# Optimization experiments

Measured on AMD Instinct MI355X. Metric: run time of the kernel, lower is better.

Reference implementation:

```python
import jax, jax.numpy as jnp
import numpy as np

BZ, C, H, W = 8, 512, 64, 64


def setup_inputs() -> dict:
    key = jax.random.key(0)
    x = jax.random.normal(key, (BZ, C, H, W), dtype=jnp.float32)
    # central square hole: flag==1 -> masked (unknown), flag==0 -> known
    mask = np.zeros((H, W), dtype=np.int32)
    mask[H // 4: 3 * H // 4, W // 4: 3 * W // 4] = 1
    return {"x": x, "mask": jnp.asarray(mask)}


def reference(x, mask):
    # InnerShiftSingle forward with shift_sz=1, stride=1, mask_thred=1:
    # flag == feature-level mask (each 1x1 patch is masked iff its pixel is masked).
    bz, c, h, w = x.shape
    c2 = c // 2
    hw = h * w
    flag = mask.reshape(hw)  # [hw] int, 1=masked, 0=known

    former = x[:, :c2]   # decoder features [b,c2,h,w]
    latter = x[:, c2:]   # encoder features [b,c2,h,w]

    former_f = former.reshape(bz, c2, hw).transpose(0, 2, 1)  # [b,hw,c2]
    latter_f = latter.reshape(bz, c2, hw).transpose(0, 2, 1)  # [b,hw,c2]

    # original: conv of (un-normalized) former with L2-normalized latter 1x1 patches
    latter_n = latter_f / (jnp.linalg.norm(latter_f, axis=-1, keepdims=True) + 1e-8)
    cosine = jnp.einsum('bpc,bqc->bpq', former_f, latter_n)  # [b,hw,hw]
    # only known-region patches (flag==0) are candidate sources
    cosine = jnp.where(flag[None, None, :] == 1, -jnp.inf, cosine)

    best = jnp.argmax(cosine, axis=-1)  # [b,hw] index into known region
    shift = jnp.take_along_axis(latter_f, best[..., None], axis=1)  # [b,hw,c2]
    # only masked positions receive a shifted feature; known positions stay 0
    shift = jnp.where(flag[None, :, None] == 1, shift, jnp.zeros((), x.dtype))
    shift = shift.transpose(0, 2, 1).reshape(bz, c2, h, w)

    return jnp.concatenate([former, latter, shift], axis=1)  # [b, 3c/2, h, w]
```

## Files before the change

### kernel.cpp

```cpp
#include <hip/hip_runtime.h>
#include <math.h>

#define BZc 8
#define Cc 512
#define C2c 256
#define HWc 4096
#define OUTC 768
#define NP 1024
#define NQ 3072
#define QG 8
#define TAU 5e-5f
#define FIXSLOTS 64

typedef _Float16 h8 __attribute__((ext_vector_type(8)));
typedef float f16v __attribute__((ext_vector_type(16)));
typedef float f32x4 __attribute__((ext_vector_type(4)));

__global__ __launch_bounds__(1024) void k_build(const int* __restrict__ mask,
                                                int* __restrict__ pidx,
                                                int* __restrict__ qinv,
                                                int* __restrict__ pinv,
                                                int* __restrict__ cnt) {
    __shared__ int s0[1024], s1[1024], t0[1024], t1[1024];
    int t = threadIdx.x;
    if (t < 8) cnt[t] = 0;
    int f[4];
    int cp = 0;
#pragma unroll
    for (int j = 0; j < 4; ++j) { f[j] = mask[t * 4 + j]; cp += f[j]; }
    s0[t] = cp; s1[t] = 4 - cp;
    __syncthreads();
    int *a = s0, *b = s1, *c = t0, *d = t1;
    for (int off = 1; off < 1024; off <<= 1) {
        int vp = a[t] + (t >= off ? a[t - off] : 0);
        int vq = b[t] + (t >= off ? b[t - off] : 0);
        c[t] = vp; d[t] = vq;
        __syncthreads();
        int* tmp;
        tmp = a; a = c; c = tmp;
        tmp = b; b = d; d = tmp;
    }
    int ep = a[t] - cp;
    int eq = b[t] - (4 - cp);
#pragma unroll
    for (int j = 0; j < 4; ++j) {
        int idx = t * 4 + j;
        if (f[j]) { pidx[ep] = idx; pinv[idx] = ep; qinv[idx] = -1; ep++; }
        else      { qinv[idx] = eq; pinv[idx] = -1; eq++; }
    }
}

__global__ __launch_bounds__(256) void k_prep(const float* __restrict__ x,
                                              const int* __restrict__ pinv,
                                              const int* __restrict__ qinv,
                                              _Float16* __restrict__ latH,
                                              _Float16* __restrict__ latL,
                                              _Float16* __restrict__ forH,
                                              _Float16* __restrict__ forL,
                                              float* __restrict__ invn,
                                              float* __restrict__ invnC,
                                              float* __restrict__ out) {
    int id = blockIdx.x;
    bool isLat = id < 1024;
    int rid = isLat ? id : id - 1024;
    int b = rid >> 7;
    int g = rid & 127;
    int col0 = g * 32;
    int tid = threadIdx.x;
    __shared__ float tile[64][33];
    __shared__ float ssq[32][33];
    __shared__ int rowm[32];
    if (tid < 32) rowm[tid] = isLat ? qinv[col0 + tid] : pinv[col0 + tid];
    const float* xb = x + (size_t)b * Cc * HWc + (isLat ? (size_t)C2c * HWc : 0);
    float* ob = out + (size_t)b * OUTC * HWc + (isLat ? (size_t)C2c * HWc : 0);
    _Float16* dH = isLat ? latH + (size_t)b * NQ * 256 : forH + (size_t)b * NP * 256;
    _Float16* dL = isLat ? latL + (size_t)b * NQ * 256 : forL + (size_t)b * NP * 256;

    int cr = tid >> 3;
    int c4 = (tid & 7) * 4;

    f32x4 vv[4][2];
#pragma unroll
    for (int c = 0; c < 4; ++c) {
        vv[c][0] = *(const f32x4*)(xb + (size_t)(c * 64 + cr) * HWc + col0 + c4);
        vv[c][1] = *(const f32x4*)(xb + (size_t)(c * 64 + 32 + cr) * HWc + col0 + c4);
    }
    __syncthreads();

    int qq = tid >> 3, sub = tid & 7;
    int dr = rowm[qq];

#pragma unroll
    for (int c = 0; c < 4; ++c) {
        int ch0 = c * 64;
        {
            f32x4 v0 = vv[c][0], v1 = vv[c][1];
            tile[cr][c4]      = v0.x; tile[cr][c4 + 1]      = v0.y;
            tile[cr][c4 + 2]  = v0.z; tile[cr][c4 + 3]      = v0.w;
            tile[32 + cr][c4] = v1.x; tile[32 + cr][c4 + 1] = v1.y;
            tile[32 + cr][c4 + 2] = v1.z; tile[32 + cr][c4 + 3] = v1.w;
        }
        __syncthreads();
        if (dr >= 0) {
            h8 hv, lv;
#pragma unroll
            for (int j = 0; j < 8; ++j) {
                float v = tile[sub * 8 + j][qq];
                _Float16 h = (_Float16)v;
                hv[j] = h; lv[j] = (_Float16)((v - (float)h) * 2048.0f);
            }
            size_t o = (size_t)dr * 256 + ch0 + sub * 8;
            *(h8*)(dH + o) = hv;
            *(h8*)(dL + o) = lv;
        }
        __syncthreads();
    }

#pragma unroll
    for (int c = 0; c < 4; ++c) {
        *(f32x4*)(ob + (size_t)(c * 64 + cr) * HWc + col0 + c4) = vv[c][0];
        *(f32x4*)(ob + (size_t)(c * 64 + 32 + cr) * HWc + col0 + c4) = vv[c][1];
    }

    if (isLat) {
        float s0 = 0.f, s1 = 0.f, s2 = 0.f, s3 = 0.f;
#pragma unroll
        for (int c = 0; c < 4; ++c)
#pragma unroll
            for (int p = 0; p < 2; ++p) {
                f32x4 v = vv[c][p];
                s0 = fmaf(v.x, v.x, s0); s1 = fmaf(v.y, v.y, s1);
                s2 = fmaf(v.z, v.z, s2); s3 = fmaf(v.w, v.w, s3);
            }
        ssq[cr][c4] = s0; ssq[cr][c4 + 1] = s1; ssq[cr][c4 + 2] = s2; ssq[cr][c4 + 3] = s3;
        __syncthreads();
        if (tid < 32) {
            float s = 0.f;
#pragma unroll
            for (int r = 0; r < 32; ++r) s += ssq[r][tid];
            float inv = 1.0f / (sqrtf(s) + 1e-8f);
            invn[b * HWc + col0 + tid] = inv;
            int qc = rowm[tid];
            if (qc >= 0) invnC[b * NQ + qc] = inv;
        }
    } else {
        f32x4 z = {0.f, 0.f, 0.f, 0.f};
        float* sb = out + (size_t)b * OUTC * HWc + (size_t)Cc * HWc;
        for (int i = tid; i < 256 * 8; i += 256) {
            int ch = i >> 3, j4 = i & 7;
            *(f32x4*)(sb + (size_t)ch * HWc + col0 + j4 * 4) = z;
        }
    }
}

__global__ __launch_bounds__(512, 2) void k_gemm(const _Float16* __restrict__ latH,
                                                 const _Float16* __restrict__ latL,
                                                 const _Float16* __restrict__ forH,
                                                 const _Float16* __restrict__ forL,
                                                 const float* __restrict__ invnC,
                                                 float* __restrict__ bv1,
                                                 int* __restrict__ bi1,
                                                 float* __restrict__ bv2) {
    int pg = blockIdx.x;
    int qg = blockIdx.y;
    int b  = blockIdx.z;
    int tid = threadIdx.x;
    int w = tid >> 6, lane = tid & 63;
    int l31 = lane & 31, lh = lane >> 5;

    __shared__ __align__(16) _Float16 sH[2][32 * 256];
    __shared__ __align__(16) _Float16 sL[2][32 * 256];
    __shared__ float sInv[384];

    if (tid < 384) sInv[tid] = invnC[b * NQ + qg * 384 + tid];

    size_t fo = ((size_t)(b * NP + pg * 256 + w * 32 + l31)) * 256 + lh * 8;
    const _Float16* fH = forH + fo;
    const _Float16* fL = forL + fo;
    h8 BH[16], BL[16];
#pragma unroll
    for (int ks = 0; ks < 16; ++ks) {
        BH[ks] = *(const h8*)(fH + ks * 16);
        BL[ks] = *(const h8*)(fL + ks * 16);
    }

    const _Float16* latHb = latH + (size_t)(b * NQ + qg * 384) * 256;
    const _Float16* latLb = latL + (size_t)(b * NQ + qg * 384) * 256;
    int sq0 = tid >> 5;
    int sq1 = 16 + (tid >> 5);
    int ssl = tid & 31;

    float v1 = -INFINITY, v2 = -INFINITY; int i1 = 0;

    f32x4 rH0, rH1, rL0, rL1;
#define LOADQ(t)                                                                   \
    rH0 = *(const f32x4*)(latHb + ((size_t)((t) * 32 + sq0) * 256 + ssl * 8));     \
    rH1 = *(const f32x4*)(latHb + ((size_t)((t) * 32 + sq1) * 256 + ssl * 8));     \
    rL0 = *(const f32x4*)(latLb + ((size_t)((t) * 32 + sq0) * 256 + ssl * 8));     \
    rL1 = *(const f32x4*)(latLb + ((size_t)((t) * 32 + sq1) * 256 + ssl * 8));
#define WRITEQ(bf)                                                                 \
    *(f32x4*)(&sH[bf][sq0 * 256 + ((ssl ^ sq0) * 8)]) = rH0;                       \
    *(f32x4*)(&sH[bf][sq1 * 256 + ((ssl ^ sq1) * 8)]) = rH1;                       \
    *(f32x4*)(&sL[bf][sq0 * 256 + ((ssl ^ sq0) * 8)]) = rL0;                       \
    *(f32x4*)(&sL[bf][sq1 * 256 + ((ssl ^ sq1) * 8)]) = rL1;

    LOADQ(0); WRITEQ(0);
    __syncthreads();

    for (int t = 0; t < 12; ++t) {
        if (t < 11) { LOADQ(t + 1); }
        const _Float16* bufH = &sH[t & 1][0];
        const _Float16* bufL = &sL[t & 1][0];
        f16v accA = {}, accB = {};
#pragma unroll
        for (int ks = 0; ks < 16; ++ks) {
            int slotA = (ks * 2 + lh) ^ l31;
            h8 aH = *(const h8*)(bufH + l31 * 256 + slotA * 8);
            h8 aL = *(const h8*)(bufL + l31 * 256 + slotA * 8);
            accA = __builtin_amdgcn_mfma_f32_32x32x16_f16(aH, BH[ks], accA, 0, 0, 0);
            accB = __builtin_amdgcn_mfma_f32_32x32x16_f16(aH, BL[ks], accB, 0, 0, 0);
            accB = __builtin_amdgcn_mfma_f32_32x32x16_f16(aL, BH[ks], accB, 0, 0, 0);
        }
#pragma unroll
        for (int r = 0; r < 16; ++r) {
            int off = (r & 3) + 8 * (r >> 2) + 4 * lh;
            float v = (accA[r] + accB[r] * (1.0f / 2048.0f)) * sInv[t * 32 + off];
            int q = qg * 384 + t * 32 + off;
            if (v > v1) { v2 = v1; v1 = v; i1 = q; }
            else if (v > v2) { v2 = v; }
        }
        if (t < 11) { WRITEQ((t + 1) & 1); }
        __syncthreads();
    }
#undef LOADQ
#undef WRITEQ
    float ov1 = __shfl_xor(v1, 32);
    int   oi1 = __shfl_xor(i1, 32);
    float ov2 = __shfl_xor(v2, 32);
    if (ov1 > v1) { v2 = fmaxf(v1, ov2); v1 = ov1; i1 = oi1; }
    else          { v2 = fmaxf(ov1, v2); }
    if (lane < 32) {
        size_t o = ((size_t)b * NP + pg * 256 + w * 32 + lane) * QG + qg;
        bv1[o] = v1; bi1[o] = i1; bv2[o] = v2;
    }
}

__global__ void k_reduce(const float* __restrict__ bv1, const int* __restrict__ bi1,
                         const float* __restrict__ bv2, int* __restrict__ bfin,
                         int* __restrict__ cnt, int* __restrict__ fixrows) {
    int t = blockIdx.x * blockDim.x + threadIdx.x;
    if (t >= BZc * NP) return;
    float V1 = -INFINITY, V2 = -INFINITY; int I1 = 0;
    for (int c = 0; c < QG; ++c) {
        float a = bv1[(size_t)t * QG + c];
        float a2 = bv2[(size_t)t * QG + c];
        int   i = bi1[(size_t)t * QG + c];
        if (a > V1) { V2 = fmaxf(V1, a2); V1 = a; I1 = i; }
        else        { V2 = fmaxf(V2, a); }
    }
    bfin[t] = I1;
    if (V1 - V2 < TAU) {
        int b = t >> 10;
        int s = atomicAdd(&cnt[b], 1);
        if (s < FIXSLOTS) fixrows[b * FIXSLOTS + s] = t & 1023;
    }
}

__global__ __launch_bounds__(256) void k_fixA(const float* __restrict__ x,
                                              const int* __restrict__ pidx,
                                              const int* __restrict__ mask,
                                              const float* __restrict__ invn,
                                              const int* __restrict__ cnt,
                                              const int* __restrict__ fixrows,
                                              float* __restrict__ fixv,
                                              int* __restrict__ fixi) {
    int qg = blockIdx.x, s = blockIdx.y, b = blockIdx.z;
    int n = cnt[b]; if (n > FIXSLOTS) n = FIXSLOTS;
    if (s >= n) return;
    int p = fixrows[b * FIXSLOTS + s];
    int porig = pidx[p];
    int tid = threadIdx.x;
    __shared__ float fs[256];
    fs[tid] = x[((size_t)b * Cc + tid) * HWc + porig];
    __syncthreads();
    const float* lx = x + ((size_t)b * Cc + C2c) * HWc;
    int q0 = qg * 1024 + tid * 4;
    float4 acc = make_float4(0.f, 0.f, 0.f, 0.f);
    for (int c0 = 0; c0 < 256; c0 += 8) {
        float4 v[8];
#pragma unroll
        for (int u = 0; u < 8; ++u)
            v[u] = *(const float4*)(lx + (size_t)(c0 + u) * HWc + q0);
#pragma unroll
        for (int u = 0; u < 8; ++u) {
            float fc = fs[c0 + u];
            acc.x = fmaf(fc, v[u].x, acc.x);
            acc.y = fmaf(fc, v[u].y, acc.y);
            acc.z = fmaf(fc, v[u].z, acc.z);
            acc.w = fmaf(fc, v[u].w, acc.w);
        }
    }
    float vals[4] = {acc.x, acc.y, acc.z, acc.w};
    float bv = -INFINITY; int bq = 1 << 30;
#pragma unroll
    for (int k = 0; k < 4; ++k) {
        int q = q0 + k;
        float val = vals[k] * invn[b * HWc + q];
        if (mask[q] == 0 && val > bv) { bv = val; bq = q; }
    }
    __shared__ float rv[256]; __shared__ int rq[256];
    rv[tid] = bv; rq[tid] = bq; __syncthreads();
    for (int off = 128; off > 0; off >>= 1) {
        if (tid < off) {
            float v2 = rv[tid + off]; int q2 = rq[tid + off];
            if (v2 > rv[tid] || (v2 == rv[tid] && q2 < rq[tid])) { rv[tid] = v2; rq[tid] = q2; }
        }
        __syncthreads();
    }
    if (tid == 0) {
        fixv[(b * FIXSLOTS + s) * 4 + qg] = rv[0];
        fixi[(b * FIXSLOTS + s) * 4 + qg] = rq[0];
    }
}

__global__ void k_fixB(const int* __restrict__ cnt, const int* __restrict__ fixrows,
                       const float* __restrict__ fixv, const int* __restrict__ fixi,
                       const int* __restrict__ qinv, int* __restrict__ bfin) {
    int t = threadIdx.x;
    int b = t >> 6, s = t & 63;
    int n = cnt[b]; if (n > FIXSLOTS) n = FIXSLOTS;
    if (s >= n) return;
    float bv = -INFINITY; int bq = 1 << 30;
    for (int qg = 0; qg < 4; ++qg) {
        float v = fixv[(b * FIXSLOTS + s) * 4 + qg];
        int   q = fixi[(b * FIXSLOTS + s) * 4 + qg];
        if (v > bv || (v == bv && q < bq)) { bv = v; bq = q; }
    }
    int p = fixrows[b * FIXSLOTS + s];
    bfin[b * NP + p] = qinv[bq];
}

__global__ __launch_bounds__(256) void k_scatter(const _Float16* __restrict__ latH,
                                                 const _Float16* __restrict__ latL,
                                                 const int* __restrict__ bfin,
                                                 const int* __restrict__ pidx,
                                                 float* __restrict__ out) {
    int blk = blockIdx.x;
    int b   = blockIdx.y;
    int tid = threadIdx.x;
    __shared__ float tile[32][257];
    __shared__ int qd[32], pd[32];
    if (tid < 32) {
        qd[tid] = bfin[b * NP + blk * 32 + tid];
        pd[tid] = pidx[blk * 32 + tid];
    }
    __syncthreads();
    for (int i = tid; i < 32 * 256; i += 256) {
        int pp = i >> 8, c = i & 255;
        size_t o = ((size_t)b * NQ + qd[pp]) * 256 + c;
        tile[pp][c] = (float)latH[o] + (float)latL[o] * (1.0f / 2048.0f);
    }
    __syncthreads();
    float* ob = out + (size_t)b * OUTC * HWc + (size_t)Cc * HWc;
    for (int i = tid; i < 256 * 32; i += 256) {
        int ch = i >> 5, j = i & 31;
        ob[(size_t)ch * HWc + pd[j]] = tile[j][ch];
    }
}

extern "C" void kernel_launch(void* const* d_in, const int* in_sizes, int n_in,
                              void* d_out, int out_size, void* d_ws, size_t ws_size,
                              hipStream_t stream) {
    const float* x    = (const float*)d_in[0];
    const int*   mask = (const int*)d_in[1];
    float* out = (float*)d_out;
    char*  ws  = (char*)d_ws;

    _Float16* latH = (_Float16*)(ws);
    _Float16* latL = (_Float16*)(ws + 12582912);
    _Float16* forH = (_Float16*)(ws + 25165824);
    _Float16* forL = (_Float16*)(ws + 29360128);
    float* invn    = (float*)(ws + 33554432);
    float* invnC   = (float*)(ws + 33685504);
    float* bv1     = (float*)(ws + 33783808);
    int*   bi1     = (int*)  (ws + 34045952);
    float* bv2     = (float*)(ws + 34308096);
    int*   bfin    = (int*)  (ws + 34570240);
    int*   pidx    = (int*)  (ws + 34603008);
    int*   qinv    = (int*)  (ws + 34607104);
    int*   pinv    = (int*)  (ws + 34623488);
    int*   cnt     = (int*)  (ws + 34639872);
    int*   fixrows = (int*)  (ws + 34639904);
    float* fixv    = (float*)(ws + 34641952);
    int*   fixi    = (int*)  (ws + 34650144);

    k_build<<<1, 1024, 0, stream>>>(mask, pidx, qinv, pinv, cnt);
    k_prep<<<2048, 256, 0, stream>>>(x, pinv, qinv, latH, latL, forH, forL, invn, invnC, out);
    k_gemm<<<dim3(4, QG, BZc), 512, 0, stream>>>(latH, latL, forH, forL, invnC, bv1, bi1, bv2);
    k_reduce<<<(BZc * NP + 255) / 256, 256, 0, stream>>>(bv1, bi1, bv2, bfin, cnt, fixrows);
    k_fixA<<<dim3(4, FIXSLOTS, BZc), 256, 0, stream>>>(x, pidx, mask, invn, cnt, fixrows, fixv, fixi);
    k_fixB<<<1, 512, 0, stream>>>(cnt, fixrows, fixv, fixi, qinv, bfin);
    k_scatter<<<dim3(32, BZc), 256, 0, stream>>>(latH, latL, bfin, pidx, out);
}
```

Before: 113.4 us.

## Pre-swizzle latent layout in global and stage tiles via direct global-to-LDS loads

The transpose kernel now writes latent fp16 hi/lo rows with the XOR slot swizzle already applied. The matmul kernel can then copy tiles straight into LDS with global_load_lds instead of going through registers, and the scatter kernel un-swizzles on read. The per-tile top-2 update also changes from a serial compare chain to a pairwise tree reduction. This removes register staging and VGPR pressure for the double buffer. It relies on the swizzle being consistent across three kernels, and async LDS writes depend on the existing barrier placement for correctness.

Measured after the change: 115.1 us. About the same (+1.4%).

```diff
diff --git a/kernel.cpp b/kernel.cpp
--- a/kernel.cpp
+++ b/kernel.cpp
@@ -15,6 +15,12 @@
 typedef _Float16 h8 __attribute__((ext_vector_type(8)));
 typedef float f16v __attribute__((ext_vector_type(16)));
 typedef float f32x4 __attribute__((ext_vector_type(4)));
+
+__device__ __forceinline__ void glds16(const void* g, void* l) {
+    __builtin_amdgcn_global_load_lds(
+        (const __attribute__((address_space(1))) void*)g,
+        (__attribute__((address_space(3))) void*)l, 16, 0, 0);
+}
 
 __global__ __launch_bounds__(1024) void k_build(const int* __restrict__ mask,
                                                 int* __restrict__ pidx,
@@ -92,7 +98,6 @@
 
 #pragma unroll
     for (int c = 0; c < 4; ++c) {
-        int ch0 = c * 64;
         {
             f32x4 v0 = vv[c][0], v1 = vv[c][1];
             tile[cr][c4]      = v0.x; tile[cr][c4 + 1]      = v0.y;
@@ -109,7 +114,9 @@
                 _Float16 h = (_Float16)v;
                 hv[j] = h; lv[j] = (_Float16)((v - (float)h) * 2048.0f);
             }
-            size_t o = (size_t)dr * 256 + ch0 + sub * 8;
+            int slot = c * 8 + sub;
+            int dslot = isLat ? (slot ^ (dr & 31)) : slot;
+            size_t o = (size_t)dr * 256 + dslot * 8;
             *(h8*)(dH + o) = hv;
             *(h8*)(dL + o) = lv;
         }
@@ -186,29 +193,29 @@
 
     const _Float16* latHb = latH + (size_t)(b * NQ + qg * 384) * 256;
     const _Float16* latLb = latL + (size_t)(b * NQ + qg * 384) * 256;
-    int sq0 = tid >> 5;
-    int sq1 = 16 + (tid >> 5);
-    int ssl = tid & 31;
-
+
+#define STAGE(bf, tt)                                                              \
+    {                                                                              \
+        const char* gH = (const char*)(latHb + (size_t)(tt) * 32 * 256);           \
+        const char* gL = (const char*)(latLb + (size_t)(tt) * 32 * 256);           \
+        char* lH = (char*)&sH[bf][0];                                              \
+        char* lL = (char*)&sL[bf][0];                                              \
+        int go = w * 2048 + lane * 16;                                             \
+        int lo = w * 2048;                                                         \
+        glds16(gH + go, lH + lo);                                                  \
+        glds16(gH + go + 1024, lH + lo + 1024);                                    \
+        glds16(gL + go, lL + lo);                                                  \
+        glds16(gL + go + 1024, lL + lo + 1024);                                    \
+    }
+
+    const int offc[16] = {0,1,2,3,8,9,10,11,16,17,18,19,24,25,26,27};
     float v1 = -INFINITY, v2 = -INFINITY; int i1 = 0;
 
-    f32x4 rH0, rH1, rL0, rL1;
-#define LOADQ(t)                                                                   \
-    rH0 = *(const f32x4*)(latHb + ((size_t)((t) * 32 + sq0) * 256 + ssl * 8));     \
-    rH1 = *(const f32x4*)(latHb + ((size_t)((t) * 32 + sq1) * 256 + ssl * 8));     \
-    rL0 = *(const f32x4*)(latLb + ((size_t)((t) * 32 + sq0) * 256 + ssl * 8));     \
-    rL1 = *(const f32x4*)(latLb + ((size_t)((t) * 32 + sq1) * 256 + ssl * 8));
-#define WRITEQ(bf)                                                                 \
-    *(f32x4*)(&sH[bf][sq0 * 256 + ((ssl ^ sq0) * 8)]) = rH0;                       \
-    *(f32x4*)(&sH[bf][sq1 * 256 + ((ssl ^ sq1) * 8)]) = rH1;                       \
-    *(f32x4*)(&sL[bf][sq0 * 256 + ((ssl ^ sq0) * 8)]) = rL0;                       \
-    *(f32x4*)(&sL[bf][sq1 * 256 + ((ssl ^ sq1) * 8)]) = rL1;
-
-    LOADQ(0); WRITEQ(0);
+    STAGE(0, 0);
     __syncthreads();
 
     for (int t = 0; t < 12; ++t) {
-        if (t < 11) { LOADQ(t + 1); }
+        if (t < 11) STAGE((t + 1) & 1, t + 1);
         const _Float16* bufH = &sH[t & 1][0];
         const _Float16* bufL = &sL[t & 1][0];
         f16v accA = {}, accB = {};
@@ -221,19 +228,42 @@
             accB = __builtin_amdgcn_mfma_f32_32x32x16_f16(aH, BL[ks], accB, 0, 0, 0);
             accB = __builtin_amdgcn_mfma_f32_32x32x16_f16(aL, BH[ks], accB, 0, 0, 0);
         }
-#pragma unroll
-        for (int r = 0; r < 16; ++r) {
-            int off = (r & 3) + 8 * (r >> 2) + 4 * lh;
-            float v = (accA[r] + accB[r] * (1.0f / 2048.0f)) * sInv[t * 32 + off];
-            int q = qg * 384 + t * 32 + off;
-            if (v > v1) { v2 = v1; v1 = v; i1 = q; }
-            else if (v > v2) { v2 = v; }
-        }
-        if (t < 11) { WRITEQ((t + 1) & 1); }
-        __syncthreads();
-    }
-#undef LOADQ
-#undef WRITEQ
+        int qb = qg * 384 + t * 32 + 4 * lh;
+        float val[16];
+#pragma unroll
+        for (int r = 0; r < 16; ++r)
+            val[r] = (accA[r] + accB[r] * (1.0f / 2048.0f)) * sInv[t * 32 + 4 * lh + offc[r]];
+        float n1[8], n2[8]; int ni[8];
+#pragma unroll
+        for (int s = 0; s < 8; ++s) {
+            float va = val[2 * s], vb = val[2 * s + 1];
+            bool bw = vb > va;
+            n1[s] = bw ? vb : va;
+            ni[s] = qb + (bw ? offc[2 * s + 1] : offc[2 * s]);
+            n2[s] = bw ? va : vb;
+        }
+#pragma unroll
+        for (int lvl = 4; lvl >= 1; lvl >>= 1) {
+#pragma unroll
+            for (int s = 0; s < 8; ++s) {
+                if (s < lvl) {
+                    float av = n1[2 * s], bv = n1[2 * s + 1];
+                    bool bw = bv > av;
+                    float m1 = bw ? bv : av;
+                    int   mi = bw ? ni[2 * s + 1] : ni[2 * s];
+                    float m2 = fmaxf(fmaxf(n2[2 * s], n2[2 * s + 1]), bw ? av : bv);
+                    n1[s] = m1; ni[s] = mi; n2[s] = m2;
+                }
+            }
+        }
+        {
+            bool bw = n1[0] > v1;
+            v2 = fmaxf(fmaxf(v2, n2[0]), bw ? v1 : n1[0]);
+            if (bw) { v1 = n1[0]; i1 = ni[0]; }
+        }
+        __syncthreads();
+    }
+#undef STAGE
     float ov1 = __shfl_xor(v1, 32);
     int   oi1 = __shfl_xor(i1, 32);
     float ov2 = __shfl_xor(v2, 32);
@@ -357,7 +387,9 @@
     __syncthreads();
     for (int i = tid; i < 32 * 256; i += 256) {
         int pp = i >> 8, c = i & 255;
-        size_t o = ((size_t)b * NQ + qd[pp]) * 256 + c;
+        int q = qd[pp];
+        int slot = c >> 3;
+        size_t o = ((size_t)b * NQ + q) * 256 + ((slot ^ (q & 31)) << 3) + (c & 7);
         tile[pp][c] = (float)latH[o] + (float)latL[o] * (1.0f / 2048.0f);
     }
     __syncthreads();
```
